# Kernel tuning notes

Measured on AMD Instinct MI355X. Metric: run time of the kernel, lower is better.

The kernel has to match this reference:

```python
import jax, jax.numpy as jnp
import numpy as np

H, DH = 8, 40            # heads, dim_head -> inner_dim = 320
SCALE = DH ** -0.5
B, N, M = 16, 4096, 77   # batch, query tokens (64x64 latent), text tokens
QD, CD, ID = 320, 768, H * DH


def setup_inputs() -> dict:
    key = jax.random.key(0)
    ks = jax.random.split(key, 7)
    x = jax.random.normal(ks[0], (B, N, QD), dtype=jnp.float32)
    context = jax.random.normal(ks[1], (B, M, CD), dtype=jnp.float32)
    # Linear weights stored as (in, out); torch nn.Linear has no bias for q/k/v
    Wq = jax.random.normal(ks[2], (QD, ID), dtype=jnp.float32) * (QD ** -0.5)
    Wk = jax.random.normal(ks[3], (CD, ID), dtype=jnp.float32) * (CD ** -0.5)
    Wv = jax.random.normal(ks[4], (CD, ID), dtype=jnp.float32) * (CD ** -0.5)
    Wo = jax.random.normal(ks[5], (ID, QD), dtype=jnp.float32) * (ID ** -0.5)
    bo = jnp.zeros((QD,), dtype=jnp.float32)
    return {"x": x, "context": context, "Wq": Wq, "Wk": Wk, "Wv": Wv, "Wo": Wo, "bo": bo}


def reference(x, context, Wq, Wk, Wv, Wo, bo):
    b, n, _ = x.shape
    m = context.shape[1]
    q = (x @ Wq).reshape(b, n, H, DH)        # to_q
    k = (context @ Wk).reshape(b, m, H, DH)  # to_k
    v = (context @ Wv).reshape(b, m, H, DH)  # to_v
    # full QK^T * scale (rank-bias path inactive: rank={} / is_add_rank=False)
    scores = jnp.einsum('bihd,bjhd->bhij', q, k) * SCALE  # [B,H,N,M]
    attn = jax.nn.softmax(scores, axis=-1)
    out = jnp.einsum('bhij,bjhd->bihd', attn, v).reshape(b, n, ID)
    return out @ Wo + bo  # to_out Linear; Dropout(p=0.0) is identity
```

## Files before the change

kernel.cpp:

```cpp
#include <hip/hip_runtime.h>

typedef unsigned short u16;
typedef unsigned int u32;
using short8 = __attribute__((ext_vector_type(8))) short;
using f32x4  = __attribute__((ext_vector_type(4))) float;

#define SCALE 0.15811388300841897f

__device__ __forceinline__ u16 f2bf(float f) {
  unsigned int u = __float_as_uint(f);
  u += 0x7fffu + ((u >> 16) & 1u);
  return (u16)(u >> 16);
}
__device__ __forceinline__ u32 pack2bf(float a, float b) {
  return (u32)f2bf(a) | ((u32)f2bf(b) << 16);
}


__global__ void prep_transpose(const float* __restrict__ Wq, const float* __restrict__ Wo,
                               const float* __restrict__ Wk, const float* __restrict__ Wv,
                               u16* __restrict__ wqt, u16* __restrict__ wot,
                               u16* __restrict__ wkt, u16* __restrict__ wvt) {
  __shared__ float ld[64][65];
  const int bid = blockIdx.x;
  const float* src; u16* dst; int K; float scale; int tk, tn;
  if (bid < 25)       { src = Wq; dst = wqt; K = 320; scale = SCALE; tk = bid / 5;         tn = bid % 5; }
  else if (bid < 50)  { src = Wo; dst = wot; K = 320; scale = 1.f;   tk = (bid - 25) / 5;  tn = (bid - 25) % 5; }
  else if (bid < 110) { src = Wk; dst = wkt; K = 768; scale = 1.f;   tk = (bid - 50) / 5;  tn = (bid - 50) % 5; }
  else                { src = Wv; dst = wvt; K = 768; scale = 1.f;   tk = (bid - 110) / 5; tn = (bid - 110) % 5; }
  const int c = threadIdx.x & 63, r0 = threadIdx.x >> 6;
  for (int rr = r0; rr < 64; rr += 4)
    ld[rr][c] = src[(size_t)(tk * 64 + rr) * 320 + tn * 64 + c];
  __syncthreads();
  for (int rr = r0; rr < 64; rr += 4)
    dst[(size_t)(tn * 64 + rr) * K + tk * 64 + c] = f2bf(ld[c][rr] * scale);
}

__global__ __launch_bounds__(256, 1)
void kv_mfma(const float* __restrict__ ctx,
             const u16* __restrict__ wkt, const u16* __restrict__ wvt,
             u16* __restrict__ kbf, u16* __restrict__ vt) {
  const int b = blockIdx.x, z = blockIdx.y;
  const int tid = threadIdx.x;
  const int w = tid >> 6, l = tid & 63, l16 = l & 15, lhi = l >> 4;
  __shared__ __align__(16) u16 sctx[80][776];

  for (int i = tid; i < 80 * 192; i += 256) {
    int row = i / 192, c4 = (i - row * 192) * 4;
    ushort4 u;
    if (row < 77) {
      float4 v = *reinterpret_cast<const float4*>(&ctx[(size_t)(b * 77 + row) * 768 + c4]);
      u.x = f2bf(v.x); u.y = f2bf(v.y); u.z = f2bf(v.z); u.w = f2bf(v.w);
    } else u = (ushort4){0, 0, 0, 0};
    *reinterpret_cast<ushort4*>(&sctx[row][c4]) = u;
  }
  if (z == 0) {
    for (int i = tid; i < 8 * 80 * 3; i += 256) {
      int hm = i / 3, q = i - hm * 3;
      int h = hm / 80, m = hm - h * 80;
      *reinterpret_cast<uint4*>(&kbf[(((size_t)b * 8 + h) * 80 + m) * 64 + 40 + q * 8]) = (uint4){0, 0, 0, 0};
    }
  } else {
    for (int i = tid; i < 8 * 48 * 2; i += 256) {
      int hd = i / 2, q = i - hd * 2;
      int h = hd / 48, d = hd - h * 48;
      *reinterpret_cast<uint4*>(&vt[(((size_t)b * 8 + h) * 48 + d) * 96 + 80 + q * 8]) = (uint4){0, 0, 0, 0};
    }
    for (int i = tid; i < 8 * 8 * 10; i += 256) {
      int h = i / 80, rem = i - h * 80;
      int d = 40 + rem / 10, q = rem - (rem / 10) * 10;
      *reinterpret_cast<uint4*>(&vt[(((size_t)b * 8 + h) * 48 + d) * 96 + q * 8]) = (uint4){0, 0, 0, 0};
    }
  }
  __syncthreads();

  f32x4 acc[5][5];
  #pragma unroll
  for (int rt = 0; rt < 5; ++rt)
    #pragma unroll
    for (int nt = 0; nt < 5; ++nt) acc[rt][nt] = (f32x4){0.f, 0.f, 0.f, 0.f};

  const u16* wbase = (z == 0 ? wkt : wvt) + (size_t)(w * 80) * 768;
  #pragma unroll 2
  for (int ks = 0; ks < 24; ++ks) {
    short8 af[5];
    #pragma unroll
    for (int rt = 0; rt < 5; ++rt)
      af[rt] = *reinterpret_cast<const short8*>(&sctx[rt * 16 + l16][ks * 32 + lhi * 8]);
    short8 bf[5];
    #pragma unroll
    for (int nt = 0; nt < 5; ++nt)
      bf[nt] = *reinterpret_cast<const short8*>(&wbase[(size_t)(nt * 16 + l16) * 768 + ks * 32 + lhi * 8]);
    #pragma unroll
    for (int rt = 0; rt < 5; ++rt)
      #pragma unroll
      for (int nt = 0; nt < 5; ++nt)
        acc[rt][nt] = __builtin_amdgcn_mfma_f32_16x16x32_bf16(af[rt], bf[nt], acc[rt][nt], 0, 0, 0);
  }

  if (z == 0) {
    #pragma unroll
    for (int rt = 0; rt < 5; ++rt)
      #pragma unroll
      for (int nt = 0; nt < 5; ++nt) {
        int c = w * 80 + nt * 16 + l16, h = c / 40, d = c - h * 40;
        #pragma unroll
        for (int r = 0; r < 4; ++r) {
          int m = rt * 16 + lhi * 4 + r;
          kbf[(((size_t)b * 8 + h) * 80 + m) * 64 + d] = f2bf(m < 77 ? acc[rt][nt][r] : 0.f);
        }
      }
  } else {
    #pragma unroll
    for (int rt = 0; rt < 5; ++rt)
      #pragma unroll
      for (int nt = 0; nt < 5; ++nt) {
        int c = w * 80 + nt * 16 + l16, h = c / 40, d = c - h * 40;
        #pragma unroll
        for (int r = 0; r < 4; ++r) {
          int m = rt * 16 + lhi * 4 + r;
          vt[(((size_t)b * 8 + h) * 48 + d) * 96 + m] = f2bf(m < 77 ? acc[rt][nt][r] : 0.f);
        }
      }
  }
}

__global__ __launch_bounds__(512, 4)
void fused(const float* __restrict__ x, const u16* __restrict__ wqt,
           const u16* __restrict__ kbf, const u16* __restrict__ vtp,
           const u16* __restrict__ wot, const float* __restrict__ bo,
           float* __restrict__ out) {
  const int bid = blockIdx.x;
  const int b  = (bid & 7) + 8 * ((bid >> 3) & 1);
  const int q0 = (bid >> 4) * 64;
  const int tid = threadIdx.x;
  const int w   = tid >> 6;
  const int l   = tid & 63;
  const int l16 = l & 15;
  const int lhi = l >> 4;
  const int w2 = w >> 2, w4 = w & 3;

  __shared__ __align__(16) u16 Qx[64][344];

  const int ctb = (w < 4) ? 3 * w : 2 * w + 4;
  int ctv[3];
  ctv[0] = ctb;
  ctv[1] = (ctb + 1 < 19) ? ctb + 1 : 19;
  ctv[2] = (ctb + 2 < 19) ? ctb + 2 : 19;

  const float4* xin = reinterpret_cast<const float4*>(x + (size_t)(b * 4096 + q0) * 320);
  for (int i = tid; i < 64 * 80; i += 512) {
    float4 v = xin[i];
    int row = i / 80, c4 = (i - row * 80) * 4;
    ushort4 u;
    u.x = f2bf(v.x); u.y = f2bf(v.y); u.z = f2bf(v.z); u.w = f2bf(v.w);
    *reinterpret_cast<ushort4*>(&Qx[row][c4]) = u;
  }
  for (int i = tid; i < 64 * 3; i += 512) {
    int row = i / 3, q = i - row * 3;
    *reinterpret_cast<uint4*>(&Qx[row][320 + q * 8]) = (uint4){0u, 0u, 0u, 0u};
  }
  __syncthreads();

  {
    f32x4 qacc[4][3];
    #pragma unroll
    for (int rt = 0; rt < 4; ++rt)
      #pragma unroll
      for (int nt = 0; nt < 3; ++nt) qacc[rt][nt] = (f32x4){0.f, 0.f, 0.f, 0.f};
    #pragma unroll
    for (int ks = 0; ks < 10; ++ks) {
      short8 af[4];
      #pragma unroll
      for (int rt = 0; rt < 4; ++rt)
        af[rt] = *reinterpret_cast<const short8*>(&Qx[rt * 16 + l16][ks * 32 + lhi * 8]);
      short8 bf[3];
      #pragma unroll
      for (int nt = 0; nt < 3; ++nt)
        bf[nt] = *reinterpret_cast<const short8*>(
            &wqt[(size_t)(ctv[nt] * 16 + l16) * 320 + ks * 32 + lhi * 8]);
      #pragma unroll
      for (int nt = 0; nt < 3; ++nt)
        #pragma unroll
        for (int rt = 0; rt < 4; ++rt)
          qacc[rt][nt] = __builtin_amdgcn_mfma_f32_16x16x32_bf16(af[rt], bf[nt], qacc[rt][nt], 0, 0, 0);
    }
    __syncthreads();
    #pragma unroll
    for (int nt = 0; nt < 3; ++nt) {
      int col = ctv[nt] * 16 + l16;
      #pragma unroll
      for (int rt = 0; rt < 4; ++rt)
        #pragma unroll
        for (int r = 0; r < 4; ++r)
          Qx[rt * 16 + lhi * 4 + r][col] = f2bf(qacc[rt][nt][r]);
    }
  }
  __syncthreads();

  {
    const int wq = w & 3, hg = w >> 2;
    const int srcLo = ((lhi & 1) << 5) + l16;
    const int srcHi = srcLo + 16;
    const bool hiSel = (lhi >= 2);

    short8 kbuf[2][5];
    {
      const u16* kh0 = kbf + (size_t)(b * 8 + hg * 4) * 80 * 64;
      #pragma unroll
      for (int mt = 0; mt < 5; ++mt)
        kbuf[0][mt] = *reinterpret_cast<const short8*>(&kh0[(mt * 16 + l16) * 64 + lhi * 8]);
    }

    #pragma unroll
    for (int hi4 = 0; hi4 < 4; ++hi4) {
      const int h = hg * 4 + hi4;
      const int cur = hi4 & 1;
      const u16* kh = kbf + (size_t)(b * 8 + h) * 80 * 64;
      const u16* vh = vtp + (size_t)(b * 8 + h) * 48 * 96;
      if (hi4 < 3) {
        const u16* khn = kh + 80 * 64;
        #pragma unroll
        for (int mt = 0; mt < 5; ++mt)
          kbuf[cur ^ 1][mt] = *reinterpret_cast<const short8*>(&khn[(mt * 16 + l16) * 64 + lhi * 8]);
      }
      short8 qk0 = *reinterpret_cast<const short8*>(&Qx[wq * 16 + l16][h * 40 + lhi * 8]);
      short8 qk1 = *reinterpret_cast<const short8*>(&Qx[wq * 16 + l16][h * 40 + 32 + lhi * 8]);
      f32x4 sacc[5];
      #pragma unroll
      for (int mt = 0; mt < 5; ++mt) sacc[mt] = (f32x4){0.f, 0.f, 0.f, 0.f};
      __builtin_amdgcn_s_setprio(1);
      #pragma unroll
      for (int mt = 0; mt < 5; ++mt) {
        sacc[mt] = __builtin_amdgcn_mfma_f32_16x16x32_bf16(kbuf[cur][mt], qk0, sacc[mt], 0, 0, 0);
        short8 ka1 = *reinterpret_cast<const short8*>(&kh[(mt * 16 + l16) * 64 + 32 + lhi * 8]);
        sacc[mt] = __builtin_amdgcn_mfma_f32_16x16x32_bf16(ka1, qk1, sacc[mt], 0, 0, 0);
      }
      __builtin_amdgcn_s_setprio(0);
      float psum = 0.f;
      #pragma unroll
      for (int mt = 0; mt < 5; ++mt)
        #pragma unroll
        for (int r = 0; r < 4; ++r) {
          float e = __expf(sacc[mt][r]);
          if (mt == 4 && lhi * 4 + r >= 13) e = 0.f;
          sacc[mt][r] = e;
          psum += e;
        }
      psum += __shfl_xor(psum, 16);
      psum += __shfl_xor(psum, 32);
      float rs = 1.f / psum;
      u32 pk[5][2];
      #pragma unroll
      for (int mt = 0; mt < 5; ++mt) {
        pk[mt][0] = pack2bf(sacc[mt][0] * rs, sacc[mt][1] * rs);
        pk[mt][1] = pack2bf(sacc[mt][2] * rs, sacc[mt][3] * rs);
      }
      uint4 fr[3];
      #pragma unroll
      for (int ks = 0; ks < 2; ++ks) {
        const int mtA = 2 * ks, mtB = 2 * ks + 1;
        u32 a0 = (u32)__shfl((int)pk[mtA][0], srcLo);
        u32 a1 = (u32)__shfl((int)pk[mtA][1], srcLo);
        u32 a2 = (u32)__shfl((int)pk[mtA][0], srcHi);
        u32 a3 = (u32)__shfl((int)pk[mtA][1], srcHi);
        u32 b0 = (u32)__shfl((int)pk[mtB][0], srcLo);
        u32 b1 = (u32)__shfl((int)pk[mtB][1], srcLo);
        u32 b2 = (u32)__shfl((int)pk[mtB][0], srcHi);
        u32 b3 = (u32)__shfl((int)pk[mtB][1], srcHi);
        fr[ks] = (uint4){hiSel ? b0 : a0, hiSel ? b1 : a1, hiSel ? b2 : a2, hiSel ? b3 : a3};
      }
      {
        u32 a0 = (u32)__shfl((int)pk[4][0], srcLo);
        u32 a1 = (u32)__shfl((int)pk[4][1], srcLo);
        u32 a2 = (u32)__shfl((int)pk[4][0], srcHi);
        u32 a3 = (u32)__shfl((int)pk[4][1], srcHi);
        fr[2] = (uint4){hiSel ? 0u : a0, hiSel ? 0u : a1, hiSel ? 0u : a2, hiSel ? 0u : a3};
      }
      f32x4 oacc[3];
      #pragma unroll
      for (int nt = 0; nt < 3; ++nt) oacc[nt] = (f32x4){0.f, 0.f, 0.f, 0.f};
      __builtin_amdgcn_s_setprio(1);
      #pragma unroll
      for (int ks = 0; ks < 3; ++ks) {
        union { uint4 u; short8 s; } cv;
        cv.u = fr[ks];
        #pragma unroll
        for (int nt = 0; nt < 3; ++nt) {
          short8 bb = *reinterpret_cast<const short8*>(&vh[(nt * 16 + l16) * 96 + ks * 32 + lhi * 8]);
          oacc[nt] = __builtin_amdgcn_mfma_f32_16x16x32_bf16(cv.s, bb, oacc[nt], 0, 0, 0);
        }
      }
      __builtin_amdgcn_s_setprio(0);
      #pragma unroll
      for (int nt = 0; nt < 3; ++nt) {
        int d = nt * 16 + l16;
        if (d < 40) {
          #pragma unroll
          for (int r = 0; r < 4; ++r)
            Qx[wq * 16 + lhi * 4 + r][h * 40 + d] = f2bf(oacc[nt][r]);
        }
      }
    }
  }
  __syncthreads();

  {
    f32x4 cacc[2][5];
    #pragma unroll
    for (int rt = 0; rt < 2; ++rt)
      #pragma unroll
      for (int nt = 0; nt < 5; ++nt) cacc[rt][nt] = (f32x4){0.f, 0.f, 0.f, 0.f};
    #pragma unroll
    for (int ks = 0; ks < 10; ++ks) {
      short8 af[2];
      #pragma unroll
      for (int rt = 0; rt < 2; ++rt)
        af[rt] = *reinterpret_cast<const short8*>(&Qx[w2 * 32 + rt * 16 + l16][ks * 32 + lhi * 8]);
      #pragma unroll
      for (int nt = 0; nt < 5; ++nt) {
        short8 bf = *reinterpret_cast<const short8*>(
            &wot[(size_t)(w4 * 80 + nt * 16 + l16) * 320 + ks * 32 + lhi * 8]);
        #pragma unroll
        for (int rt = 0; rt < 2; ++rt)
          cacc[rt][nt] = __builtin_amdgcn_mfma_f32_16x16x32_bf16(af[rt], bf, cacc[rt][nt], 0, 0, 0);
      }
    }
    #pragma unroll
    for (int nt = 0; nt < 5; ++nt) {
      int col = w4 * 80 + nt * 16 + l16;
      float bias = bo[col];
      #pragma unroll
      for (int rt = 0; rt < 2; ++rt) {
        #pragma unroll
        for (int r = 0; r < 4; ++r) {
          int row = w2 * 32 + rt * 16 + lhi * 4 + r;
          out[(size_t)(b * 4096 + q0 + row) * 320 + col] = cacc[rt][nt][r] + bias;
        }
      }
    }
  }
}

extern "C" void kernel_launch(void* const* d_in, const int* in_sizes, int n_in,
                              void* d_out, int out_size, void* d_ws, size_t ws_size,
                              hipStream_t stream) {
  (void)in_sizes; (void)n_in; (void)out_size; (void)ws_size;
  const float* x       = (const float*)d_in[0];
  const float* context = (const float*)d_in[1];
  const float* Wq      = (const float*)d_in[2];
  const float* Wk      = (const float*)d_in[3];
  const float* Wv      = (const float*)d_in[4];
  const float* Wo      = (const float*)d_in[5];
  const float* bo      = (const float*)d_in[6];
  float* out = (float*)d_out;
  u16* ws = (u16*)d_ws;
  u16* wqt = ws;
  u16* wot = ws + 102400;
  u16* wkt = ws + 204800;
  u16* wvt = ws + 450560;
  u16* kbf = ws + 696320;
  u16* vtp = ws + 1351680;

  prep_transpose<<<170, 256, 0, stream>>>(Wq, Wo, Wk, Wv, wqt, wot, wkt, wvt);
  kv_mfma<<<dim3(16, 2), 256, 0, stream>>>(context, wkt, wvt, kbf, vtp);
  fused<<<1024, 512, 0, stream>>>(x, wqt, kbf, vtp, wot, bo, out);
}
```

Baseline: 186.6 us.

## Halve fused block to 32 query rows with 4 waves and double grid

Shrinks each fused block from 64 query rows and 8 waves to 32 rows and 4 waves, launching 2048 blocks instead of 1024. Each wave now owns 5 Q-projection column tiles and 80 output columns, and the attention phase maps 2 head groups of 4 heads across the waves. The aim is more blocks for better load balance and occupancy with a smaller LDS footprint. The cost is that weight tiles (Wq, Wo) and per-head K/V are re-read by twice as many blocks.

```diff
diff --git a/kernel.cpp b/kernel.cpp
--- a/kernel.cpp
+++ b/kernel.cpp
@@ -125,72 +125,63 @@
   }
 }
 
-__global__ __launch_bounds__(512, 4)
+__global__ __launch_bounds__(256, 4)
 void fused(const float* __restrict__ x, const u16* __restrict__ wqt,
            const u16* __restrict__ kbf, const u16* __restrict__ vtp,
            const u16* __restrict__ wot, const float* __restrict__ bo,
            float* __restrict__ out) {
   const int bid = blockIdx.x;
   const int b  = (bid & 7) + 8 * ((bid >> 3) & 1);
-  const int q0 = (bid >> 4) * 64;
+  const int q0 = (bid >> 4) * 32;
   const int tid = threadIdx.x;
   const int w   = tid >> 6;
   const int l   = tid & 63;
   const int l16 = l & 15;
   const int lhi = l >> 4;
-  const int w2 = w >> 2, w4 = w & 3;
-
-  __shared__ __align__(16) u16 Qx[64][344];
-
-  const int ctb = (w < 4) ? 3 * w : 2 * w + 4;
-  int ctv[3];
-  ctv[0] = ctb;
-  ctv[1] = (ctb + 1 < 19) ? ctb + 1 : 19;
-  ctv[2] = (ctb + 2 < 19) ? ctb + 2 : 19;
+
+  __shared__ __align__(16) u16 Qx[32][344];
 
   const float4* xin = reinterpret_cast<const float4*>(x + (size_t)(b * 4096 + q0) * 320);
-  for (int i = tid; i < 64 * 80; i += 512) {
+  for (int i = tid; i < 32 * 80; i += 256) {
     float4 v = xin[i];
     int row = i / 80, c4 = (i - row * 80) * 4;
     ushort4 u;
     u.x = f2bf(v.x); u.y = f2bf(v.y); u.z = f2bf(v.z); u.w = f2bf(v.w);
     *reinterpret_cast<ushort4*>(&Qx[row][c4]) = u;
   }
-  for (int i = tid; i < 64 * 3; i += 512) {
-    int row = i / 3, q = i - row * 3;
+  if (tid < 32 * 3) {
+    int row = tid / 3, q = tid - row * 3;
     *reinterpret_cast<uint4*>(&Qx[row][320 + q * 8]) = (uint4){0u, 0u, 0u, 0u};
   }
   __syncthreads();
 
   {
-    f32x4 qacc[4][3];
-    #pragma unroll
-    for (int rt = 0; rt < 4; ++rt)
-      #pragma unroll
-      for (int nt = 0; nt < 3; ++nt) qacc[rt][nt] = (f32x4){0.f, 0.f, 0.f, 0.f};
+    f32x4 qacc[2][5];
+    #pragma unroll
+    for (int rt = 0; rt < 2; ++rt)
+      #pragma unroll
+      for (int nt = 0; nt < 5; ++nt) qacc[rt][nt] = (f32x4){0.f, 0.f, 0.f, 0.f};
     #pragma unroll
     for (int ks = 0; ks < 10; ++ks) {
-      short8 af[4];
-      #pragma unroll
-      for (int rt = 0; rt < 4; ++rt)
+      short8 af[2];
+      #pragma unroll
+      for (int rt = 0; rt < 2; ++rt)
         af[rt] = *reinterpret_cast<const short8*>(&Qx[rt * 16 + l16][ks * 32 + lhi * 8]);
-      short8 bf[3];
-      #pragma unroll
-      for (int nt = 0; nt < 3; ++nt)
-        bf[nt] = *reinterpret_cast<const short8*>(
-            &wqt[(size_t)(ctv[nt] * 16 + l16) * 320 + ks * 32 + lhi * 8]);
-      #pragma unroll
-      for (int nt = 0; nt < 3; ++nt)
-        #pragma unroll
-        for (int rt = 0; rt < 4; ++rt)
-          qacc[rt][nt] = __builtin_amdgcn_mfma_f32_16x16x32_bf16(af[rt], bf[nt], qacc[rt][nt], 0, 0, 0);
+      #pragma unroll
+      for (int nt = 0; nt < 5; ++nt) {
+        short8 bf = *reinterpret_cast<const short8*>(
+            &wqt[(size_t)((w * 5 + nt) * 16 + l16) * 320 + ks * 32 + lhi * 8]);
+        #pragma unroll
+        for (int rt = 0; rt < 2; ++rt)
+          qacc[rt][nt] = __builtin_amdgcn_mfma_f32_16x16x32_bf16(af[rt], bf, qacc[rt][nt], 0, 0, 0);
+      }
     }
     __syncthreads();
     #pragma unroll
-    for (int nt = 0; nt < 3; ++nt) {
-      int col = ctv[nt] * 16 + l16;
-      #pragma unroll
-      for (int rt = 0; rt < 4; ++rt)
+    for (int nt = 0; nt < 5; ++nt) {
+      int col = (w * 5 + nt) * 16 + l16;
+      #pragma unroll
+      for (int rt = 0; rt < 2; ++rt)
         #pragma unroll
         for (int r = 0; r < 4; ++r)
           Qx[rt * 16 + lhi * 4 + r][col] = f2bf(qacc[rt][nt][r]);
@@ -199,7 +190,7 @@
   __syncthreads();
 
   {
-    const int wq = w & 3, hg = w >> 2;
+    const int wq = w & 1, hg = w >> 1;
     const int srcLo = ((lhi & 1) << 5) + l16;
     const int srcHi = srcLo + 16;
     const bool hiSel = (lhi >= 2);
@@ -316,11 +307,11 @@
       short8 af[2];
       #pragma unroll
       for (int rt = 0; rt < 2; ++rt)
-        af[rt] = *reinterpret_cast<const short8*>(&Qx[w2 * 32 + rt * 16 + l16][ks * 32 + lhi * 8]);
+        af[rt] = *reinterpret_cast<const short8*>(&Qx[rt * 16 + l16][ks * 32 + lhi * 8]);
       #pragma unroll
       for (int nt = 0; nt < 5; ++nt) {
         short8 bf = *reinterpret_cast<const short8*>(
-            &wot[(size_t)(w4 * 80 + nt * 16 + l16) * 320 + ks * 32 + lhi * 8]);
+            &wot[(size_t)(w * 80 + nt * 16 + l16) * 320 + ks * 32 + lhi * 8]);
         #pragma unroll
         for (int rt = 0; rt < 2; ++rt)
           cacc[rt][nt] = __builtin_amdgcn_mfma_f32_16x16x32_bf16(af[rt], bf, cacc[rt][nt], 0, 0, 0);
@@ -328,13 +319,13 @@
     }
     #pragma unroll
     for (int nt = 0; nt < 5; ++nt) {
-      int col = w4 * 80 + nt * 16 + l16;
+      int col = w * 80 + nt * 16 + l16;
       float bias = bo[col];
       #pragma unroll
       for (int rt = 0; rt < 2; ++rt) {
         #pragma unroll
         for (int r = 0; r < 4; ++r) {
-          int row = w2 * 32 + rt * 16 + lhi * 4 + r;
+          int row = rt * 16 + lhi * 4 + r;
           out[(size_t)(b * 4096 + q0 + row) * 320 + col] = cacc[rt][nt][r] + bias;
         }
       }
@@ -364,5 +355,5 @@
 
   prep_transpose<<<170, 256, 0, stream>>>(Wq, Wo, Wk, Wv, wqt, wot, wkt, wvt);
   kv_mfma<<<dim3(16, 2), 256, 0, stream>>>(context, wkt, wvt, kbf, vtp);
-  fused<<<1024, 512, 0, stream>>>(x, wqt, kbf, vtp, wot, bo, out);
-}
+  fused<<<2048, 256, 0, stream>>>(x, wqt, kbf, vtp, wot, bo, out);
+}
```

Result: slower. 208.3 us (+11.6%).

## Process two query tiles per block and prefetch next x tile into registers

Applied to the files above, without the earlier changes.

The fused kernel becomes persistent-ish: the grid is halved and each block loops over two 64-row query tiles. The x tile for the second iteration is loaded into registers while the first tile runs, so global load latency overlaps with compute. This adds 40 registers of float4 buffering, which could pressure occupancy under launch_bounds(512,4). It also halves the number of blocks, so fewer waves can hide latency.

```diff
diff --git a/kernel.cpp b/kernel.cpp
--- a/kernel.cpp
+++ b/kernel.cpp
@@ -130,9 +130,6 @@
            const u16* __restrict__ kbf, const u16* __restrict__ vtp,
            const u16* __restrict__ wot, const float* __restrict__ bo,
            float* __restrict__ out) {
-  const int bid = blockIdx.x;
-  const int b  = (bid & 7) + 8 * ((bid >> 3) & 1);
-  const int q0 = (bid >> 4) * 64;
   const int tid = threadIdx.x;
   const int w   = tid >> 6;
   const int l   = tid & 63;
@@ -148,197 +145,224 @@
   ctv[1] = (ctb + 1 < 19) ? ctb + 1 : 19;
   ctv[2] = (ctb + 2 < 19) ? ctb + 2 : 19;
 
-  const float4* xin = reinterpret_cast<const float4*>(x + (size_t)(b * 4096 + q0) * 320);
-  for (int i = tid; i < 64 * 80; i += 512) {
-    float4 v = xin[i];
-    int row = i / 80, c4 = (i - row * 80) * 4;
-    ushort4 u;
-    u.x = f2bf(v.x); u.y = f2bf(v.y); u.z = f2bf(v.z); u.w = f2bf(v.w);
-    *reinterpret_cast<ushort4*>(&Qx[row][c4]) = u;
-  }
   for (int i = tid; i < 64 * 3; i += 512) {
     int row = i / 3, q = i - row * 3;
     *reinterpret_cast<uint4*>(&Qx[row][320 + q * 8]) = (uint4){0u, 0u, 0u, 0u};
   }
-  __syncthreads();
-
+
+  float4 xbuf[10];
   {
-    f32x4 qacc[4][3];
-    #pragma unroll
-    for (int rt = 0; rt < 4; ++rt)
-      #pragma unroll
-      for (int nt = 0; nt < 3; ++nt) qacc[rt][nt] = (f32x4){0.f, 0.f, 0.f, 0.f};
-    #pragma unroll
-    for (int ks = 0; ks < 10; ++ks) {
-      short8 af[4];
+    const int g = blockIdx.x;
+    const int b = (g & 7) + 8 * ((g >> 3) & 1);
+    const int q0 = (g >> 4) * 64;
+    const float4* xin = reinterpret_cast<const float4*>(x + (size_t)(b * 4096 + q0) * 320);
+    #pragma unroll
+    for (int k = 0; k < 10; ++k) xbuf[k] = xin[tid + k * 512];
+  }
+
+  for (int tau = 0; tau < 2; ++tau) {
+    const int g = blockIdx.x + tau * 512;
+    const int b = (g & 7) + 8 * ((g >> 3) & 1);
+    const int q0 = (g >> 4) * 64;
+
+    #pragma unroll
+    for (int k = 0; k < 10; ++k) {
+      int i = tid + k * 512;
+      int row = i / 80, c4 = (i - row * 80) * 4;
+      ushort4 u;
+      u.x = f2bf(xbuf[k].x); u.y = f2bf(xbuf[k].y);
+      u.z = f2bf(xbuf[k].z); u.w = f2bf(xbuf[k].w);
+      *reinterpret_cast<ushort4*>(&Qx[row][c4]) = u;
+    }
+    if (tau == 0) {
+      const int g2 = blockIdx.x + 512;
+      const int b2 = (g2 & 7) + 8 * ((g2 >> 3) & 1);
+      const int q02 = (g2 >> 4) * 64;
+      const float4* xin2 = reinterpret_cast<const float4*>(x + (size_t)(b2 * 4096 + q02) * 320);
+      #pragma unroll
+      for (int k = 0; k < 10; ++k) xbuf[k] = xin2[tid + k * 512];
+    }
+    __syncthreads();
+
+    {
+      f32x4 qacc[4][3];
       #pragma unroll
       for (int rt = 0; rt < 4; ++rt)
-        af[rt] = *reinterpret_cast<const short8*>(&Qx[rt * 16 + l16][ks * 32 + lhi * 8]);
-      short8 bf[3];
-      #pragma unroll
-      for (int nt = 0; nt < 3; ++nt)
-        bf[nt] = *reinterpret_cast<const short8*>(
-            &wqt[(size_t)(ctv[nt] * 16 + l16) * 320 + ks * 32 + lhi * 8]);
-      #pragma unroll
-      for (int nt = 0; nt < 3; ++nt)
+        #pragma unroll
+        for (int nt = 0; nt < 3; ++nt) qacc[rt][nt] = (f32x4){0.f, 0.f, 0.f, 0.f};
+      #pragma unroll
+      for (int ks = 0; ks < 10; ++ks) {
+        short8 af[4];
         #pragma unroll
         for (int rt = 0; rt < 4; ++rt)
-          qacc[rt][nt] = __builtin_amdgcn_mfma_f32_16x16x32_bf16(af[rt], bf[nt], qacc[rt][nt], 0, 0, 0);
+          af[rt] = *reinterpret_cast<const short8*>(&Qx[rt * 16 + l16][ks * 32 + lhi * 8]);
+        short8 bf[3];
+        #pragma unroll
+        for (int nt = 0; nt < 3; ++nt)
+          bf[nt] = *reinterpret_cast<const short8*>(
+              &wqt[(size_t)(ctv[nt] * 16 + l16) * 320 + ks * 32 + lhi * 8]);
+        #pragma unroll
+        for (int nt = 0; nt < 3; ++nt)
+          #pragma unroll
+          for (int rt = 0; rt < 4; ++rt)
+            qacc[rt][nt] = __builtin_amdgcn_mfma_f32_16x16x32_bf16(af[rt], bf[nt], qacc[rt][nt], 0, 0, 0);
+      }
+      __syncthreads();
+      #pragma unroll
+      for (int nt = 0; nt < 3; ++nt) {
+        int col = ctv[nt] * 16 + l16;
+        #pragma unroll
+        for (int rt = 0; rt < 4; ++rt)
+          #pragma unroll
+          for (int r = 0; r < 4; ++r)
+            Qx[rt * 16 + lhi * 4 + r][col] = f2bf(qacc[rt][nt][r]);
+      }
     }
     __syncthreads();
-    #pragma unroll
-    for (int nt = 0; nt < 3; ++nt) {
-      int col = ctv[nt] * 16 + l16;
-      #pragma unroll
-      for (int rt = 0; rt < 4; ++rt)
-        #pragma unroll
-        for (int r = 0; r < 4; ++r)
-          Qx[rt * 16 + lhi * 4 + r][col] = f2bf(qacc[rt][nt][r]);
-    }
-  }
-  __syncthreads();
-
-  {
-    const int wq = w & 3, hg = w >> 2;
-    const int srcLo = ((lhi & 1) << 5) + l16;
-    const int srcHi = srcLo + 16;
-    const bool hiSel = (lhi >= 2);
-
-    short8 kbuf[2][5];
+
     {
-      const u16* kh0 = kbf + (size_t)(b * 8 + hg * 4) * 80 * 64;
-      #pragma unroll
-      for (int mt = 0; mt < 5; ++mt)
-        kbuf[0][mt] = *reinterpret_cast<const short8*>(&kh0[(mt * 16 + l16) * 64 + lhi * 8]);
-    }
-
-    #pragma unroll
-    for (int hi4 = 0; hi4 < 4; ++hi4) {
-      const int h = hg * 4 + hi4;
-      const int cur = hi4 & 1;
-      const u16* kh = kbf + (size_t)(b * 8 + h) * 80 * 64;
-      const u16* vh = vtp + (size_t)(b * 8 + h) * 48 * 96;
-      if (hi4 < 3) {
-        const u16* khn = kh + 80 * 64;
+      const int wq = w & 3, hg = w >> 2;
+      const int srcLo = ((lhi & 1) << 5) + l16;
+      const int srcHi = srcLo + 16;
+      const bool hiSel = (lhi >= 2);
+
+      short8 kbuf[2][5];
+      {
+        const u16* kh0 = kbf + (size_t)(b * 8 + hg * 4) * 80 * 64;
         #pragma unroll
         for (int mt = 0; mt < 5; ++mt)
-          kbuf[cur ^ 1][mt] = *reinterpret_cast<const short8*>(&khn[(mt * 16 + l16) * 64 + lhi * 8]);
-      }
-      short8 qk0 = *reinterpret_cast<const short8*>(&Qx[wq * 16 + l16][h * 40 + lhi * 8]);
-      short8 qk1 = *reinterpret_cast<const short8*>(&Qx[wq * 16 + l16][h * 40 + 32 + lhi * 8]);
-      f32x4 sacc[5];
-      #pragma unroll
-      for (int mt = 0; mt < 5; ++mt) sacc[mt] = (f32x4){0.f, 0.f, 0.f, 0.f};
-      __builtin_amdgcn_s_setprio(1);
-      #pragma unroll
-      for (int mt = 0; mt < 5; ++mt) {
-        sacc[mt] = __builtin_amdgcn_mfma_f32_16x16x32_bf16(kbuf[cur][mt], qk0, sacc[mt], 0, 0, 0);
-        short8 ka1 = *reinterpret_cast<const short8*>(&kh[(mt * 16 + l16) * 64 + 32 + lhi * 8]);
-        sacc[mt] = __builtin_amdgcn_mfma_f32_16x16x32_bf16(ka1, qk1, sacc[mt], 0, 0, 0);
-      }
-      __builtin_amdgcn_s_setprio(0);
-      float psum = 0.f;
-      #pragma unroll
-      for (int mt = 0; mt < 5; ++mt)
-        #pragma unroll
-        for (int r = 0; r < 4; ++r) {
-          float e = __expf(sacc[mt][r]);
-          if (mt == 4 && lhi * 4 + r >= 13) e = 0.f;
-          sacc[mt][r] = e;
-          psum += e;
-        }
-      psum += __shfl_xor(psum, 16);
-      psum += __shfl_xor(psum, 32);
-      float rs = 1.f / psum;
-      u32 pk[5][2];
-      #pragma unroll
-      for (int mt = 0; mt < 5; ++mt) {
-        pk[mt][0] = pack2bf(sacc[mt][0] * rs, sacc[mt][1] * rs);
-        pk[mt][1] = pack2bf(sacc[mt][2] * rs, sacc[mt][3] * rs);
-      }
-      uint4 fr[3];
-      #pragma unroll
-      for (int ks = 0; ks < 2; ++ks) {
-        const int mtA = 2 * ks, mtB = 2 * ks + 1;
-        u32 a0 = (u32)__shfl((int)pk[mtA][0], srcLo);
-        u32 a1 = (u32)__shfl((int)pk[mtA][1], srcLo);
-        u32 a2 = (u32)__shfl((int)pk[mtA][0], srcHi);
-        u32 a3 = (u32)__shfl((int)pk[mtA][1], srcHi);
-        u32 b0 = (u32)__shfl((int)pk[mtB][0], srcLo);
-        u32 b1 = (u32)__shfl((int)pk[mtB][1], srcLo);
-        u32 b2 = (u32)__shfl((int)pk[mtB][0], srcHi);
-        u32 b3 = (u32)__shfl((int)pk[mtB][1], srcHi);
-        fr[ks] = (uint4){hiSel ? b0 : a0, hiSel ? b1 : a1, hiSel ? b2 : a2, hiSel ? b3 : a3};
-      }
-      {
-        u32 a0 = (u32)__shfl((int)pk[4][0], srcLo);
-        u32 a1 = (u32)__shfl((int)pk[4][1], srcLo);
-        u32 a2 = (u32)__shfl((int)pk[4][0], srcHi);
-        u32 a3 = (u32)__shfl((int)pk[4][1], srcHi);
-        fr[2] = (uint4){hiSel ? 0u : a0, hiSel ? 0u : a1, hiSel ? 0u : a2, hiSel ? 0u : a3};
-      }
-      f32x4 oacc[3];
-      #pragma unroll
-      for (int nt = 0; nt < 3; ++nt) oacc[nt] = (f32x4){0.f, 0.f, 0.f, 0.f};
-      __builtin_amdgcn_s_setprio(1);
-      #pragma unroll
-      for (int ks = 0; ks < 3; ++ks) {
-        union { uint4 u; short8 s; } cv;
-        cv.u = fr[ks];
+          kbuf[0][mt] = *reinterpret_cast<const short8*>(&kh0[(mt * 16 + l16) * 64 + lhi * 8]);
+      }
+
+      #pragma unroll
+      for (int hi4 = 0; hi4 < 4; ++hi4) {
+        const int h = hg * 4 + hi4;
+        const int cur = hi4 & 1;
+        const u16* kh = kbf + (size_t)(b * 8 + h) * 80 * 64;
+        const u16* vh = vtp + (size_t)(b * 8 + h) * 48 * 96;
+        if (hi4 < 3) {
+          const u16* khn = kh + 80 * 64;
+          #pragma unroll
+          for (int mt = 0; mt < 5; ++mt)
+            kbuf[cur ^ 1][mt] = *reinterpret_cast<const short8*>(&khn[(mt * 16 + l16) * 64 + lhi * 8]);
+        }
+        short8 qk0 = *reinterpret_cast<const short8*>(&Qx[wq * 16 + l16][h * 40 + lhi * 8]);
+        short8 qk1 = *reinterpret_cast<const short8*>(&Qx[wq * 16 + l16][h * 40 + 32 + lhi * 8]);
+        f32x4 sacc[5];
+        #pragma unroll
+        for (int mt = 0; mt < 5; ++mt) sacc[mt] = (f32x4){0.f, 0.f, 0.f, 0.f};
+        __builtin_amdgcn_s_setprio(1);
+        #pragma unroll
+        for (int mt = 0; mt < 5; ++mt) {
+          sacc[mt] = __builtin_amdgcn_mfma_f32_16x16x32_bf16(kbuf[cur][mt], qk0, sacc[mt], 0, 0, 0);
+          short8 ka1 = *reinterpret_cast<const short8*>(&kh[(mt * 16 + l16) * 64 + 32 + lhi * 8]);
+          sacc[mt] = __builtin_amdgcn_mfma_f32_16x16x32_bf16(ka1, qk1, sacc[mt], 0, 0, 0);
+        }
+        __builtin_amdgcn_s_setprio(0);
+        float psum = 0.f;
+        #pragma unroll
+        for (int mt = 0; mt < 5; ++mt)
+          #pragma unroll
+          for (int r = 0; r < 4; ++r) {
+            float e = __expf(sacc[mt][r]);
+            if (mt == 4 && lhi * 4 + r >= 13) e = 0.f;
+            sacc[mt][r] = e;
+            psum += e;
+          }
+        psum += __shfl_xor(psum, 16);
+        psum += __shfl_xor(psum, 32);
+        float rs = 1.f / psum;
+        u32 pk[5][2];
+        #pragma unroll
+        for (int mt = 0; mt < 5; ++mt) {
+          pk[mt][0] = pack2bf(sacc[mt][0] * rs, sacc[mt][1] * rs);
+          pk[mt][1] = pack2bf(sacc[mt][2] * rs, sacc[mt][3] * rs);
+        }
+        uint4 fr[3];
+        #pragma unroll
+        for (int ks = 0; ks < 2; ++ks) {
+          const int mtA = 2 * ks, mtB = 2 * ks + 1;
+          u32 a0 = (u32)__shfl((int)pk[mtA][0], srcLo);
+          u32 a1 = (u32)__shfl((int)pk[mtA][1], srcLo);
+          u32 a2 = (u32)__shfl((int)pk[mtA][0], srcHi);
+          u32 a3 = (u32)__shfl((int)pk[mtA][1], srcHi);
+          u32 b0 = (u32)__shfl((int)pk[mtB][0], srcLo);
+          u32 b1 = (u32)__shfl((int)pk[mtB][1], srcLo);
+          u32 b2 = (u32)__shfl((int)pk[mtB][0], srcHi);
+          u32 b3 = (u32)__shfl((int)pk[mtB][1], srcHi);
+          fr[ks] = (uint4){hiSel ? b0 : a0, hiSel ? b1 : a1, hiSel ? b2 : a2, hiSel ? b3 : a3};
+        }
+        {
+          u32 a0 = (u32)__shfl((int)pk[4][0], srcLo);
+          u32 a1 = (u32)__shfl((int)pk[4][1], srcLo);
+          u32 a2 = (u32)__shfl((int)pk[4][0], srcHi);
+          u32 a3 = (u32)__shfl((int)pk[4][1], srcHi);
+          fr[2] = (uint4){hiSel ? 0u : a0, hiSel ? 0u : a1, hiSel ? 0u : a2, hiSel ? 0u : a3};
+        }
+        f32x4 oacc[3];
+        #pragma unroll
+        for (int nt = 0; nt < 3; ++nt) oacc[nt] = (f32x4){0.f, 0.f, 0.f, 0.f};
+        __builtin_amdgcn_s_setprio(1);
+        #pragma unroll
+        for (int ks = 0; ks < 3; ++ks) {
+          union { uint4 u; short8 s; } cv;
+          cv.u = fr[ks];
+          #pragma unroll
+          for (int nt = 0; nt < 3; ++nt) {
+            short8 bb = *reinterpret_cast<const short8*>(&vh[(nt * 16 + l16) * 96 + ks * 32 + lhi * 8]);
+            oacc[nt] = __builtin_amdgcn_mfma_f32_16x16x32_bf16(cv.s, bb, oacc[nt], 0, 0, 0);
+          }
+        }
+        __builtin_amdgcn_s_setprio(0);
         #pragma unroll
         for (int nt = 0; nt < 3; ++nt) {
-          short8 bb = *reinterpret_cast<const short8*>(&vh[(nt * 16 + l16) * 96 + ks * 32 + lhi * 8]);
-          oacc[nt] = __builtin_amdgcn_mfma_f32_16x16x32_bf16(cv.s, bb, oacc[nt], 0, 0, 0);
-        }
-      }
-      __builtin_amdgcn_s_setprio(0);
-      #pragma unroll
-      for (int nt = 0; nt < 3; ++nt) {
-        int d = nt * 16 + l16;
-        if (d < 40) {
-          #pragma unroll
-          for (int r = 0; r < 4; ++r)
-            Qx[wq * 16 + lhi * 4 + r][h * 40 + d] = f2bf(oacc[nt][r]);
-        }
-      }
-    }
-  }
-  __syncthreads();
-
-  {
-    f32x4 cacc[2][5];
-    #pragma unroll
-    for (int rt = 0; rt < 2; ++rt)
-      #pragma unroll
-      for (int nt = 0; nt < 5; ++nt) cacc[rt][nt] = (f32x4){0.f, 0.f, 0.f, 0.f};
-    #pragma unroll
-    for (int ks = 0; ks < 10; ++ks) {
-      short8 af[2];
+          int d = nt * 16 + l16;
+          if (d < 40) {
+            #pragma unroll
+            for (int r = 0; r < 4; ++r)
+              Qx[wq * 16 + lhi * 4 + r][h * 40 + d] = f2bf(oacc[nt][r]);
+          }
+        }
+      }
+    }
+    __syncthreads();
+
+    {
+      f32x4 cacc[2][5];
       #pragma unroll
       for (int rt = 0; rt < 2; ++rt)
-        af[rt] = *reinterpret_cast<const short8*>(&Qx[w2 * 32 + rt * 16 + l16][ks * 32 + lhi * 8]);
+        #pragma unroll
+        for (int nt = 0; nt < 5; ++nt) cacc[rt][nt] = (f32x4){0.f, 0.f, 0.f, 0.f};
+      #pragma unroll
+      for (int ks = 0; ks < 10; ++ks) {
+        short8 af[2];
+        #pragma unroll
+        for (int rt = 0; rt < 2; ++rt)
+          af[rt] = *reinterpret_cast<const short8*>(&Qx[w2 * 32 + rt * 16 + l16][ks * 32 + lhi * 8]);
+        #pragma unroll
+        for (int nt = 0; nt < 5; ++nt) {
+          short8 bf = *reinterpret_cast<const short8*>(
+              &wot[(size_t)(w4 * 80 + nt * 16 + l16) * 320 + ks * 32 + lhi * 8]);
+          #pragma unroll
+          for (int rt = 0; rt < 2; ++rt)
+            cacc[rt][nt] = __builtin_amdgcn_mfma_f32_16x16x32_bf16(af[rt], bf, cacc[rt][nt], 0, 0, 0);
+        }
+      }
       #pragma unroll
       for (int nt = 0; nt < 5; ++nt) {
-        short8 bf = *reinterpret_cast<const short8*>(
-            &wot[(size_t)(w4 * 80 + nt * 16 + l16) * 320 + ks * 32 + lhi * 8]);
-        #pragma unroll
-        for (int rt = 0; rt < 2; ++rt)
-          cacc[rt][nt] = __builtin_amdgcn_mfma_f32_16x16x32_bf16(af[rt], bf, cacc[rt][nt], 0, 0, 0);
-      }
-    }
-    #pragma unroll
-    for (int nt = 0; nt < 5; ++nt) {
-      int col = w4 * 80 + nt * 16 + l16;
-      float bias = bo[col];
-      #pragma unroll
-      for (int rt = 0; rt < 2; ++rt) {
-        #pragma unroll
-        for (int r = 0; r < 4; ++r) {
-          int row = w2 * 32 + rt * 16 + lhi * 4 + r;
-          out[(size_t)(b * 4096 + q0 + row) * 320 + col] = cacc[rt][nt][r] + bias;
-        }
-      }
-    }
+        int col = w4 * 80 + nt * 16 + l16;
+        float bias = bo[col];
+        #pragma unroll
+        for (int rt = 0; rt < 2; ++rt) {
+          #pragma unroll
+          for (int r = 0; r < 4; ++r) {
+            int row = w2 * 32 + rt * 16 + lhi * 4 + r;
+            out[(size_t)(b * 4096 + q0 + row) * 320 + col] = cacc[rt][nt][r] + bias;
+          }
+        }
+      }
+    }
+    __syncthreads();
   }
 }
 
@@ -364,5 +388,5 @@
 
   prep_transpose<<<170, 256, 0, stream>>>(Wq, Wo, Wk, Wv, wqt, wot, wkt, wvt);
   kv_mfma<<<dim3(16, 2), 256, 0, stream>>>(context, wkt, wvt, kbf, vtp);
-  fused<<<1024, 512, 0, stream>>>(x, wqt, kbf, vtp, wot, bo, out);
-}
+  fused<<<512, 512, 0, stream>>>(x, wqt, kbf, vtp, wot, bo, out);
+}
```

Result: slower. 681.2 us (+265.0%).
